# Optimization experiments

Measured on AMD Instinct MI355X. Metric: run time of the kernel, lower is better.

Reference implementation:

```python
import jax, jax.numpy as jnp
import numpy as np

DIM = 256
HEADS = 8


def _ln(x, g, b, eps=1e-5):
    mu = jnp.mean(x, axis=-1, keepdims=True)
    var = jnp.var(x, axis=-1, keepdims=True)
    return (x - mu) * jax.lax.rsqrt(var + eps) * g + b


def setup_inputs() -> dict:
    key = jax.random.key(0)
    ks = jax.random.split(key, 12)
    d = DIM
    s = lambda fan: 1.0 / np.sqrt(fan)
    return {
        "x": jax.random.normal(ks[0], (1, d, 64, 64), dtype=jnp.float32),
        "ln1_g": jnp.ones((d,), jnp.float32),
        "ln1_b": jnp.zeros((d,), jnp.float32),
        "w_qkv": jax.random.normal(ks[1], (3 * d, d), jnp.float32) * s(d),
        "b_qkv": jnp.zeros((3 * d,), jnp.float32),
        "w_proj": jax.random.normal(ks[2], (d, d), jnp.float32) * s(d),
        "b_proj": jnp.zeros((d,), jnp.float32),
        "ln2_g": jnp.ones((d,), jnp.float32),
        "ln2_b": jnp.zeros((d,), jnp.float32),
        "w_mlp1": jax.random.normal(ks[3], (4 * d, d), jnp.float32) * s(d),
        "b_mlp1": jnp.zeros((4 * d,), jnp.float32),
        "w_mlp2": jax.random.normal(ks[4], (d, 4 * d), jnp.float32) * s(4 * d),
        "b_mlp2": jnp.zeros((d,), jnp.float32),
    }


def reference(x, ln1_g, ln1_b, w_qkv, b_qkv, w_proj, b_proj,
              ln2_g, ln2_b, w_mlp1, b_mlp1, w_mlp2, b_mlp2):
    B, C, H, W = x.shape
    hd = HEADS
    d = C // hd
    scale = d ** (-0.5)
    # work channels-last: [B, H, W, C] -> [B, HW, C]
    xl = jnp.transpose(x, (0, 2, 3, 1)).reshape(B, H * W, C)

    # --- attention branch ---
    xn = _ln(xl, ln1_g, ln1_b)
    qkv = jnp.einsum('bnc,oc->bno', xn, w_qkv) + b_qkv  # [B, N, 3C]
    q, k, v = jnp.split(qkv, 3, axis=-1)
    def heads(t):  # [B,N,C] -> [B,h,N,d]
        return jnp.transpose(t.reshape(B, H * W, hd, d), (0, 2, 1, 3))
    q, k, v = heads(q), heads(k), heads(v)
    attn = jax.nn.softmax(jnp.einsum('bhnd,bhmd->bhnm', q, k) * scale, axis=-1)
    out = jnp.einsum('bhnm,bhmd->bhnd', attn, v)  # [B,h,N,d]
    out = jnp.transpose(out, (0, 2, 1, 3)).reshape(B, H * W, C)
    xl = xl + jnp.einsum('bnc,oc->bno', out, w_proj) + b_proj

    # --- MLP branch ---
    xn = _ln(xl, ln2_g, ln2_b)
    h1 = jax.nn.gelu(jnp.einsum('bnc,oc->bno', xn, w_mlp1) + b_mlp1,
                     approximate=False)
    xl = xl + jnp.einsum('bnf,of->bno', h1, w_mlp2) + b_mlp2

    return jnp.transpose(xl.reshape(B, H, W, C), (0, 3, 1, 2))
```

## Files before the change

### kernel.cpp

```cpp
#include <hip/hip_runtime.h>
#include <hip/hip_bf16.h>

typedef __bf16 bf16_t;
typedef __bf16 bf16x8 __attribute__((ext_vector_type(8)));
typedef __bf16 bf16x4 __attribute__((ext_vector_type(4)));
typedef float  f32x4  __attribute__((ext_vector_type(4)));

#define MFMA(a,b,c) __builtin_amdgcn_mfma_f32_16x16x32_bf16((a),(b),(c),0,0,0)

__device__ __forceinline__ size_t pidx(int n, int k, int K) {
  return (size_t)(n >> 4) * (K << 4) + ((k >> 3) << 7) + ((n & 15) << 3) + (k & 7);
}

__global__ __launch_bounds__(256) void cvt_pack_all(const float* __restrict__ w_qkv,
                                                    const float* __restrict__ w_proj,
                                                    const float* __restrict__ w_mlp1,
                                                    const float* __restrict__ w_mlp2,
                                                    bf16_t* __restrict__ wq, bf16_t* __restrict__ wp,
                                                    bf16_t* __restrict__ w1, bf16_t* __restrict__ w2) {
  int b = blockIdx.x;
  const float* src; bf16_t* dst; int t0, ksh;
  if (b < 96)       { src = w_qkv;  dst = wq; ksh = 5; t0 = b * 256; }
  else if (b < 128) { src = w_proj; dst = wp; ksh = 5; t0 = (b - 96) * 256; }
  else if (b < 256) { src = w_mlp1; dst = w1; ksh = 5; t0 = (b - 128) * 256; }
  else              { src = w_mlp2; dst = w2; ksh = 7; t0 = (b - 256) * 256; }
  int t = t0 + threadIdx.x;
  int n = t >> ksh, kb = t & ((1 << ksh) - 1);
  int K = 8 << ksh;
  const float* p = src + (size_t)n * K + kb * 8;
  float4 a = *(const float4*)p;
  float4 c = *(const float4*)(p + 4);
  bf16x8 o = {(bf16_t)a.x, (bf16_t)a.y, (bf16_t)a.z, (bf16_t)a.w,
              (bf16_t)c.x, (bf16_t)c.y, (bf16_t)c.z, (bf16_t)c.w};
  *(bf16x8*)(dst + (size_t)(n >> 4) * (K << 4) + kb * 128 + ((n & 15) << 3)) = o;
}

__global__ __launch_bounds__(256) void fused_in(const float* __restrict__ x,
                                                const float* __restrict__ g,
                                                const float* __restrict__ bta,
                                                float* __restrict__ xl,
                                                bf16_t* __restrict__ xn) {
  __shared__ float tile[256][33];
  __shared__ float psum[8][32], psq[8][32], mu_s[32], rs_s[32];
  int t = threadIdx.x, n0 = blockIdx.x * 32;
  int lane32 = t & 31, grp = t >> 5;
#pragma unroll
  for (int it = 0; it < 32; ++it) {
    int c = grp + it * 8;
    tile[c][lane32] = x[(size_t)c * 4096 + n0 + lane32];
  }
  __syncthreads();
  float s = 0.f, sq = 0.f;
#pragma unroll
  for (int ci = 0; ci < 32; ++ci) {
    float v = tile[grp * 32 + ci][lane32];
    s += v; sq += v * v;
  }
  psum[grp][lane32] = s; psq[grp][lane32] = sq;
  __syncthreads();
  if (t < 32) {
    float S = 0.f, Q = 0.f;
#pragma unroll
    for (int p = 0; p < 8; ++p) { S += psum[p][t]; Q += psq[p][t]; }
    float mu = S * (1.0f / 256.0f);
    float var = Q * (1.0f / 256.0f) - mu * mu;
    mu_s[t] = mu; rs_s[t] = rsqrtf(var + 1e-5f);
  }
  __syncthreads();
  {
    float mu = mu_s[lane32], rs = rs_s[lane32];
    int row = n0 + lane32;
    bf16_t* op = xn + (size_t)(row >> 4) * 4096 + ((row & 15) << 3);
#pragma unroll
    for (int cc8 = 0; cc8 < 4; ++cc8) {
      int c0 = grp * 32 + cc8 * 8;
      bf16x8 o;
#pragma unroll
      for (int j = 0; j < 8; ++j) {
        int c = c0 + j;
        o[j] = (bf16_t)((tile[c][lane32] - mu) * rs * g[c] + bta[c]);
      }
      *(bf16x8*)(op + ((c0 >> 3) << 7)) = o;
    }
  }
#pragma unroll
  for (int it = 0; it < 4; ++it) {
    int j = grp + it * 8;
#pragma unroll
    for (int c0 = 0; c0 < 256; c0 += 32)
      xl[(size_t)(n0 + j) * 256 + c0 + lane32] = tile[c0 + lane32][j];
  }
}

template <int K, int EPI, int RPW, int KS = 1>
__global__ __launch_bounds__(256) void gemm_bt(const bf16_t* __restrict__ A,
                                               const bf16_t* __restrict__ W,
                                               const float* __restrict__ bias,
                                               void* __restrict__ outp, int ldn) {
  constexpr int RB = RPW / 16;
  constexpr int KLEN = K / KS;
  int w = threadIdx.x >> 6, lane = threadIdx.x & 63;
  int quad = lane >> 4, idx = lane & 15;
  int row0 = blockIdx.x * (4 * RPW) + w * RPW;
  int col0 = blockIdx.y * 64;
  int kb0 = (KS > 1) ? blockIdx.z * KLEN : 0;
  f32x4 acc[RB][4];
#pragma unroll
  for (int rb = 0; rb < RB; ++rb)
#pragma unroll
    for (int nb = 0; nb < 4; ++nb) acc[rb][nb] = (f32x4){0.f, 0.f, 0.f, 0.f};
  const bf16_t* abase = A + (size_t)(row0 >> 4) * (K << 4) + quad * 128 + idx * 8;
  const bf16_t* wbase = W + (size_t)(col0 >> 4) * (K << 4) + quad * 128 + idx * 8;
#pragma unroll 4
  for (int k0 = kb0; k0 < kb0 + KLEN; k0 += 32) {
    bf16x8 a[RB];
#pragma unroll
    for (int rb = 0; rb < RB; ++rb)
      a[rb] = *(const bf16x8*)(abase + (size_t)rb * (K << 4) + k0 * 16);
#pragma unroll
    for (int nb = 0; nb < 4; ++nb) {
      bf16x8 b = *(const bf16x8*)(wbase + (size_t)nb * (K << 4) + k0 * 16);
#pragma unroll
      for (int rb = 0; rb < RB; ++rb) acc[rb][nb] = MFMA(a[rb], b, acc[rb][nb]);
    }
  }
#pragma unroll
  for (int nb = 0; nb < 4; ++nb) {
    int c = col0 + nb * 16 + idx;
    float bv = (EPI == 4) ? 0.f : bias[c];
#pragma unroll
    for (int rb = 0; rb < RB; ++rb)
#pragma unroll
      for (int r = 0; r < 4; ++r) {
        int rr = row0 + rb * 16 + quad * 4 + r;
        float v = acc[rb][nb][r] + bv;
        if constexpr (EPI == 1) {
          v = 0.5f * v * (1.0f + erff(v * 0.70710678118654752f));
          ((bf16_t*)outp)[pidx(rr, c, ldn)] = (bf16_t)v;
        } else if constexpr (EPI == 4) {
          ((float*)outp)[((size_t)blockIdx.z * 4096 + rr) * ldn + c] = v;
        } else {
          bf16_t* qh = (bf16_t*)outp;
          bf16_t* kh = qh + 1048576;
          bf16_t* vp = kh + 1048576;
          if (c < 256) {
            qh[(size_t)(c >> 5) * 131072 + rr * 32 + (c & 31)] = (bf16_t)v;
          } else if (c < 512) {
            kh[(size_t)((c - 256) >> 5) * 131072 + rr * 32 + (c & 31)] = (bf16_t)v;
          } else {
            vp[(size_t)((c - 512) >> 5) * 131072 + (rr >> 5) * 1024 + (c & 31) * 32 + (rr & 31)] = (bf16_t)v;
          }
        }
      }
  }
}

#define SPLIT 4
__global__ __launch_bounds__(256, 4) void attn_split(const bf16_t* __restrict__ qkvh,
                                                     bf16_t* __restrict__ o_part,
                                                     float* __restrict__ l_part) {
  __shared__ bf16_t P[4][32][72];
  int w = threadIdx.x >> 6, lane = threadIdx.x & 63;
  int quad = lane >> 4, idx = lane & 15;
  int qt = blockIdx.x & 31;
  int h  = (blockIdx.x >> 5) & 7;
  int sp = blockIdx.x >> 8;
  int qrow = qt * 128 + w * 32;
  const bf16_t* qh = qkvh + (size_t)h * 131072;
  const bf16_t* kh = qh + 8 * 131072;
  const bf16_t* vp = kh + 8 * 131072;
  const float cs = 0.25503518f;
  bf16x8 qr0 = *(const bf16x8*)(qh + (size_t)(qrow + idx) * 32 + quad * 8);
  bf16x8 qr1 = *(const bf16x8*)(qh + (size_t)(qrow + 16 + idx) * 32 + quad * 8);
  bf16x8 qf0, qf1;
#pragma unroll
  for (int j = 0; j < 8; ++j) {
    qf0[j] = (bf16_t)((float)qr0[j] * cs);
    qf1[j] = (bf16_t)((float)qr1[j] * cs);
  }
  float ls0 = 0.f, ls1 = 0.f;
  f32x4 o00 = {0.f,0.f,0.f,0.f}, o01 = {0.f,0.f,0.f,0.f};
  f32x4 o10 = {0.f,0.f,0.f,0.f}, o11 = {0.f,0.f,0.f,0.f};
  const f32x4 zero = {0.f,0.f,0.f,0.f};
  int kbase = sp * 1024;

  bf16x8 kf[4];
#pragma unroll
  for (int kb = 0; kb < 4; ++kb)
    kf[kb] = *(const bf16x8*)(kh + (size_t)(kbase + kb * 16 + idx) * 32 + quad * 8);

  for (int kt = 0; kt < 16; ++kt) {
    int k0 = kbase + kt * 64;
    int k1 = kbase + ((kt + 1) & 15) * 64;
    const bf16_t* vt = vp + (size_t)(k0 >> 5) * 1024 + quad * 8;
    bf16x8 vv0 = *(const bf16x8*)(vt + idx * 32);
    bf16x8 vv1 = *(const bf16x8*)(vt + (idx + 16) * 32);
    bf16x8 vv2 = *(const bf16x8*)(vt + 1024 + idx * 32);
    bf16x8 vv3 = *(const bf16x8*)(vt + 1024 + (idx + 16) * 32);
    bf16x8 kfn[4];
#pragma unroll
    for (int kb = 0; kb < 4; ++kb)
      kfn[kb] = *(const bf16x8*)(kh + (size_t)(k1 + kb * 16 + idx) * 32 + quad * 8);
#pragma unroll
    for (int kb = 0; kb < 4; ++kb) {
      f32x4 s0 = MFMA(kf[kb], qf0, zero);
      f32x4 s1 = MFMA(kf[kb], qf1, zero);
      float a0 = __builtin_amdgcn_exp2f(s0[0]), a1 = __builtin_amdgcn_exp2f(s0[1]);
      float a2 = __builtin_amdgcn_exp2f(s0[2]), a3 = __builtin_amdgcn_exp2f(s0[3]);
      float b0 = __builtin_amdgcn_exp2f(s1[0]), b1 = __builtin_amdgcn_exp2f(s1[1]);
      float b2 = __builtin_amdgcn_exp2f(s1[2]), b3 = __builtin_amdgcn_exp2f(s1[3]);
      ls0 += (a0 + a1) + (a2 + a3);
      ls1 += (b0 + b1) + (b2 + b3);
      bf16x4 pk0 = {(bf16_t)a0, (bf16_t)a1, (bf16_t)a2, (bf16_t)a3};
      bf16x4 pk1 = {(bf16_t)b0, (bf16_t)b1, (bf16_t)b2, (bf16_t)b3};
      *(bf16x4*)&P[w][idx][kb * 16 + quad * 4] = pk0;
      *(bf16x4*)&P[w][16 + idx][kb * 16 + quad * 4] = pk1;
    }
#pragma unroll
    for (int kc = 0; kc < 2; ++kc) {
      bf16x8 pa0 = *(const bf16x8*)&P[w][idx][kc * 32 + quad * 8];
      bf16x8 pa1 = *(const bf16x8*)&P[w][16 + idx][kc * 32 + quad * 8];
      bf16x8 va = kc ? vv2 : vv0;
      bf16x8 vb = kc ? vv3 : vv1;
      o00 = MFMA(pa0, va, o00);
      o01 = MFMA(pa0, vb, o01);
      o10 = MFMA(pa1, va, o10);
      o11 = MFMA(pa1, vb, o11);
    }
#pragma unroll
    for (int kb = 0; kb < 4; ++kb) kf[kb] = kfn[kb];
  }
  ls0 += __shfl_xor(ls0, 16); ls0 += __shfl_xor(ls0, 32);
  ls1 += __shfl_xor(ls1, 16); ls1 += __shfl_xor(ls1, 32);
  if (quad == 0) {
    l_part[((size_t)sp * 8 + h) * 4096 + qrow + idx]      = ls0;
    l_part[((size_t)sp * 8 + h) * 4096 + qrow + 16 + idx] = ls1;
  }
#pragma unroll
  for (int r = 0; r < 4; ++r) {
    int n0 = qrow + quad * 4 + r;
    size_t b0a = ((size_t)sp * 4096 + n0) * 256 + h * 32;
    o_part[b0a + idx]      = (bf16_t)o00[r];
    o_part[b0a + 16 + idx] = (bf16_t)o01[r];
    size_t b1a = b0a + 16 * 256;
    o_part[b1a + idx]      = (bf16_t)o10[r];
    o_part[b1a + 16 + idx] = (bf16_t)o11[r];
  }
}

__global__ __launch_bounds__(256) void attn_norm(const bf16_t* __restrict__ o_part,
                                                 const float* __restrict__ l_part,
                                                 bf16_t* __restrict__ attn) {
  int i = (blockIdx.x * 256 + threadIdx.x) * 4;
  int n = i >> 8, cc = i & 255, h = cc >> 5;
  float l = 0.f;
#pragma unroll
  for (int s = 0; s < SPLIT; ++s) l += l_part[((size_t)s * 8 + h) * 4096 + n];
  float inv = 1.0f / l;
  float acc[4] = {0.f, 0.f, 0.f, 0.f};
#pragma unroll
  for (int s = 0; s < SPLIT; ++s) {
    bf16x4 v = *(const bf16x4*)(o_part + ((size_t)s * 4096 + n) * 256 + cc);
#pragma unroll
    for (int j = 0; j < 4; ++j) acc[j] += (float)v[j];
  }
  bf16x4 o = {(bf16_t)(acc[0] * inv), (bf16_t)(acc[1] * inv),
              (bf16_t)(acc[2] * inv), (bf16_t)(acc[3] * inv)};
  *(bf16x4*)(attn + (size_t)(n >> 4) * 4096 + ((cc >> 3) << 7) + ((n & 15) << 3) + (cc & 7)) = o;
}

__global__ __launch_bounds__(256) void combine_ln(const float* __restrict__ pp,
                                                  const float* __restrict__ xl,
                                                  const float* __restrict__ bias,
                                                  const float* __restrict__ g,
                                                  const float* __restrict__ bta,
                                                  float* __restrict__ xl2,
                                                  bf16_t* __restrict__ xn2) {
  int row  = blockIdx.x * 4 + (threadIdx.x >> 6);
  int lane = threadIdx.x & 63;
  size_t ri = (size_t)row * 64 + lane;
  float4 p0 = ((const float4*)pp)[ri];
  float4 p1 = ((const float4*)pp)[ri + 4096 * 64];
  float4 rr = ((const float4*)xl)[ri];
  float4 bb = ((const float4*)bias)[lane];
  float4 v = {p0.x + p1.x + rr.x + bb.x, p0.y + p1.y + rr.y + bb.y,
              p0.z + p1.z + rr.z + bb.z, p0.w + p1.w + rr.w + bb.w};
  ((float4*)xl2)[ri] = v;
  float s  = v.x + v.y + v.z + v.w;
  float sq = v.x * v.x + v.y * v.y + v.z * v.z + v.w * v.w;
#pragma unroll
  for (int off = 32; off; off >>= 1) {
    s  += __shfl_xor(s, off);
    sq += __shfl_xor(sq, off);
  }
  float mu  = s * (1.0f / 256.0f);
  float var = sq * (1.0f / 256.0f) - mu * mu;
  float rs  = rsqrtf(var + 1e-5f);
  float4 gg = ((const float4*)g)[lane];
  float4 b2 = ((const float4*)bta)[lane];
  bf16x4 o = {(bf16_t)((v.x - mu) * rs * gg.x + b2.x),
              (bf16_t)((v.y - mu) * rs * gg.y + b2.y),
              (bf16_t)((v.z - mu) * rs * gg.z + b2.z),
              (bf16_t)((v.w - mu) * rs * gg.w + b2.w)};
  int k = lane * 4;
  *(bf16x4*)(xn2 + (size_t)(row >> 4) * 4096 + ((k >> 3) << 7) + ((row & 15) << 3) + (k & 7)) = o;
}

__global__ __launch_bounds__(256) void combine_transpose(const float* __restrict__ mp,
                                                         const float* __restrict__ xl2,
                                                         const float* __restrict__ bias,
                                                         float* __restrict__ dst) {
  __shared__ float tile[32][33];
  int n0 = blockIdx.x * 32, c0 = blockIdx.y * 32;
  int a = threadIdx.x & 31, b = threadIdx.x >> 5;
  float bv = bias[c0 + a];
#pragma unroll
  for (int i = 0; i < 4; ++i) {
    int n = b + i * 8;
    size_t base = (size_t)(n0 + n) * 256 + c0 + a;
    float v = xl2[base] + bv;
#pragma unroll
    for (int s = 0; s < 4; ++s) v += mp[(size_t)s * 1048576 + base];
    tile[a][n] = v;
  }
  __syncthreads();
#pragma unroll
  for (int i = 0; i < 4; ++i) {
    int c = b + i * 8;
    dst[(size_t)(c0 + c) * 4096 + n0 + a] = tile[c][a];
  }
}

extern "C" void kernel_launch(void* const* d_in, const int* in_sizes, int n_in,
                              void* d_out, int out_size, void* d_ws, size_t ws_size,
                              hipStream_t stream) {
  const float* x      = (const float*)d_in[0];
  const float* ln1_g  = (const float*)d_in[1];
  const float* ln1_b  = (const float*)d_in[2];
  const float* w_qkv  = (const float*)d_in[3];
  const float* b_qkv  = (const float*)d_in[4];
  const float* w_proj = (const float*)d_in[5];
  const float* b_proj = (const float*)d_in[6];
  const float* ln2_g  = (const float*)d_in[7];
  const float* ln2_b  = (const float*)d_in[8];
  const float* w_mlp1 = (const float*)d_in[9];
  const float* b_mlp1 = (const float*)d_in[10];
  const float* w_mlp2 = (const float*)d_in[11];
  const float* b_mlp2 = (const float*)d_in[12];

  char* ws = (char*)d_ws;
  bf16_t* qkvh   = (bf16_t*)(ws + 0);
  float*  xl     = (float*)(ws + (6u << 20));
  bf16_t* xn     = (bf16_t*)(ws + (10u << 20));
  bf16_t* o_part = (bf16_t*)(ws + (12u << 20));
  bf16_t* attn   = (bf16_t*)(ws + (20u << 20));
  bf16_t* wq     = (bf16_t*)(ws + (22u << 20));
  bf16_t* wp     = wq + 196608;
  bf16_t* w1     = wp + 65536;
  bf16_t* w2     = w1 + 262144;
  float*  l_part = (float*)(ws + (24064u << 10));
  float*  pp     = (float*)(ws + (24u << 20));
  float*  xl2    = (float*)(ws + (10u << 20));
  bf16_t* xn2    = (bf16_t*)(ws + (14u << 20));
  bf16_t* h1     = (bf16_t*)(ws + 0);
  float*  mp     = (float*)(ws + (24u << 20));

  cvt_pack_all<<<384, 256, 0, stream>>>(w_qkv, w_proj, w_mlp1, w_mlp2, wq, wp, w1, w2);
  fused_in<<<128, 256, 0, stream>>>(x, ln1_g, ln1_b, xl, xn);

  gemm_bt<256, 3, 16><<<dim3(64, 12), 256, 0, stream>>>(xn, wq, b_qkv, qkvh, 768);
  attn_split<<<256 * SPLIT, 256, 0, stream>>>(qkvh, o_part, l_part);
  attn_norm<<<1024, 256, 0, stream>>>(o_part, l_part, attn);

  gemm_bt<256, 4, 16, 2><<<dim3(64, 4, 2), 256, 0, stream>>>(attn, wp, nullptr, pp, 256);
  combine_ln<<<1024, 256, 0, stream>>>(pp, xl, b_proj, ln2_g, ln2_b, xl2, xn2);

  gemm_bt<256, 1, 16><<<dim3(64, 16), 256, 0, stream>>>(xn2, w1, b_mlp1, h1, 1024);
  gemm_bt<1024, 4, 16, 4><<<dim3(64, 4, 4), 256, 0, stream>>>(h1, w2, nullptr, mp, 256);
  combine_transpose<<<dim3(128, 8), 256, 0, stream>>>(mp, xl2, b_mlp2, (float*)d_out);
}
```

Before: 169.5 us.

## Software-pipeline attention P tiles, pack o_part stores, tanh-approx GELU, relocate buffers

Attention now double-buffers the P tile in shared memory and computes the next tile's QK^T and exp before the current PV MFMAs, so softmax math overlaps the PV matmuls. Partial outputs are stored as packed bf16 pairs in 32-bit words, and attn_norm reads them with 128-bit loads using half the threads. The erf GELU is replaced with a tanh approximation built from exp2 and rcp, and workspace buffers are moved around. The tanh GELU differs numerically from the exact erf form, and the double buffer doubles shared memory per block.

Measured after the change: 176.8 us. +4.3%, slower.

```diff
diff --git a/kernel.cpp b/kernel.cpp
--- a/kernel.cpp
+++ b/kernel.cpp
@@ -5,11 +5,18 @@
 typedef __bf16 bf16x8 __attribute__((ext_vector_type(8)));
 typedef __bf16 bf16x4 __attribute__((ext_vector_type(4)));
 typedef float  f32x4  __attribute__((ext_vector_type(4)));
+typedef unsigned int uint;
 
 #define MFMA(a,b,c) __builtin_amdgcn_mfma_f32_16x16x32_bf16((a),(b),(c),0,0,0)
 
 __device__ __forceinline__ size_t pidx(int n, int k, int K) {
   return (size_t)(n >> 4) * (K << 4) + ((k >> 3) << 7) + ((n & 15) << 3) + (k & 7);
+}
+
+__device__ __forceinline__ uint packbf2(float lo, float hi) {
+  unsigned short a = __builtin_bit_cast(unsigned short, (bf16_t)lo);
+  unsigned short b = __builtin_bit_cast(unsigned short, (bf16_t)hi);
+  return (uint)a | ((uint)b << 16);
 }
 
 __global__ __launch_bounds__(256) void cvt_pack_all(const float* __restrict__ w_qkv,
@@ -135,7 +142,10 @@
         int rr = row0 + rb * 16 + quad * 4 + r;
         float v = acc[rb][nb][r] + bv;
         if constexpr (EPI == 1) {
-          v = 0.5f * v * (1.0f + erff(v * 0.70710678118654752f));
+          float z = v * (0.7978845608f + 0.0356774081f * v * v);
+          float t = __builtin_amdgcn_exp2f(z * 2.885390082f);
+          float th = 1.f - 2.f * __builtin_amdgcn_rcpf(t + 1.f);
+          v = 0.5f * v * (1.f + th);
           ((bf16_t*)outp)[pidx(rr, c, ldn)] = (bf16_t)v;
         } else if constexpr (EPI == 4) {
           ((float*)outp)[((size_t)blockIdx.z * 4096 + rr) * ldn + c] = v;
@@ -157,9 +167,9 @@
 
 #define SPLIT 4
 __global__ __launch_bounds__(256, 4) void attn_split(const bf16_t* __restrict__ qkvh,
-                                                     bf16_t* __restrict__ o_part,
+                                                     uint* __restrict__ o_part,
                                                      float* __restrict__ l_part) {
-  __shared__ bf16_t P[4][32][72];
+  __shared__ bf16_t P[2][4][32][72];
   int w = threadIdx.x >> 6, lane = threadIdx.x & 63;
   int quad = lane >> 4, idx = lane & 15;
   int qt = blockIdx.x & 31;
@@ -189,44 +199,68 @@
   for (int kb = 0; kb < 4; ++kb)
     kf[kb] = *(const bf16x8*)(kh + (size_t)(kbase + kb * 16 + idx) * 32 + quad * 8);
 
-  for (int kt = 0; kt < 16; ++kt) {
-    int k0 = kbase + kt * 64;
-    int k1 = kbase + ((kt + 1) & 15) * 64;
+#pragma unroll
+  for (int kb = 0; kb < 4; ++kb) {
+    f32x4 s0 = MFMA(kf[kb], qf0, zero);
+    f32x4 s1 = MFMA(kf[kb], qf1, zero);
+    float a0 = __builtin_amdgcn_exp2f(s0[0]), a1 = __builtin_amdgcn_exp2f(s0[1]);
+    float a2 = __builtin_amdgcn_exp2f(s0[2]), a3 = __builtin_amdgcn_exp2f(s0[3]);
+    float b0 = __builtin_amdgcn_exp2f(s1[0]), b1 = __builtin_amdgcn_exp2f(s1[1]);
+    float b2 = __builtin_amdgcn_exp2f(s1[2]), b3 = __builtin_amdgcn_exp2f(s1[3]);
+    ls0 += (a0 + a1) + (a2 + a3);
+    ls1 += (b0 + b1) + (b2 + b3);
+    bf16x4 pk0 = {(bf16_t)a0, (bf16_t)a1, (bf16_t)a2, (bf16_t)a3};
+    bf16x4 pk1 = {(bf16_t)b0, (bf16_t)b1, (bf16_t)b2, (bf16_t)b3};
+    *(bf16x4*)&P[0][w][idx][kb * 16 + quad * 4] = pk0;
+    *(bf16x4*)&P[0][w][16 + idx][kb * 16 + quad * 4] = pk1;
+  }
+#pragma unroll
+  for (int kb = 0; kb < 4; ++kb)
+    kf[kb] = *(const bf16x8*)(kh + (size_t)(kbase + 64 + kb * 16 + idx) * 32 + quad * 8);
+
+#pragma unroll 2
+  for (int t = 0; t < 16; ++t) {
+    int par = t & 1;
+    int k0 = kbase + t * 64;
+    bf16x8 pa00 = *(const bf16x8*)&P[par][w][idx][quad * 8];
+    bf16x8 pa01 = *(const bf16x8*)&P[par][w][idx][32 + quad * 8];
+    bf16x8 pa10 = *(const bf16x8*)&P[par][w][16 + idx][quad * 8];
+    bf16x8 pa11 = *(const bf16x8*)&P[par][w][16 + idx][32 + quad * 8];
     const bf16_t* vt = vp + (size_t)(k0 >> 5) * 1024 + quad * 8;
     bf16x8 vv0 = *(const bf16x8*)(vt + idx * 32);
     bf16x8 vv1 = *(const bf16x8*)(vt + (idx + 16) * 32);
     bf16x8 vv2 = *(const bf16x8*)(vt + 1024 + idx * 32);
     bf16x8 vv3 = *(const bf16x8*)(vt + 1024 + (idx + 16) * 32);
+    int kn = kbase + ((t + 2) & 15) * 64;
     bf16x8 kfn[4];
 #pragma unroll
     for (int kb = 0; kb < 4; ++kb)
-      kfn[kb] = *(const bf16x8*)(kh + (size_t)(k1 + kb * 16 + idx) * 32 + quad * 8);
-#pragma unroll
-    for (int kb = 0; kb < 4; ++kb) {
-      f32x4 s0 = MFMA(kf[kb], qf0, zero);
-      f32x4 s1 = MFMA(kf[kb], qf1, zero);
-      float a0 = __builtin_amdgcn_exp2f(s0[0]), a1 = __builtin_amdgcn_exp2f(s0[1]);
-      float a2 = __builtin_amdgcn_exp2f(s0[2]), a3 = __builtin_amdgcn_exp2f(s0[3]);
-      float b0 = __builtin_amdgcn_exp2f(s1[0]), b1 = __builtin_amdgcn_exp2f(s1[1]);
-      float b2 = __builtin_amdgcn_exp2f(s1[2]), b3 = __builtin_amdgcn_exp2f(s1[3]);
-      ls0 += (a0 + a1) + (a2 + a3);
-      ls1 += (b0 + b1) + (b2 + b3);
-      bf16x4 pk0 = {(bf16_t)a0, (bf16_t)a1, (bf16_t)a2, (bf16_t)a3};
-      bf16x4 pk1 = {(bf16_t)b0, (bf16_t)b1, (bf16_t)b2, (bf16_t)b3};
-      *(bf16x4*)&P[w][idx][kb * 16 + quad * 4] = pk0;
-      *(bf16x4*)&P[w][16 + idx][kb * 16 + quad * 4] = pk1;
+      kfn[kb] = *(const bf16x8*)(kh + (size_t)(kn + kb * 16 + idx) * 32 + quad * 8);
+    if (t < 15) {
+#pragma unroll
+      for (int kb = 0; kb < 4; ++kb) {
+        f32x4 s0 = MFMA(kf[kb], qf0, zero);
+        f32x4 s1 = MFMA(kf[kb], qf1, zero);
+        float a0 = __builtin_amdgcn_exp2f(s0[0]), a1 = __builtin_amdgcn_exp2f(s0[1]);
+        float a2 = __builtin_amdgcn_exp2f(s0[2]), a3 = __builtin_amdgcn_exp2f(s0[3]);
+        float b0 = __builtin_amdgcn_exp2f(s1[0]), b1 = __builtin_amdgcn_exp2f(s1[1]);
+        float b2 = __builtin_amdgcn_exp2f(s1[2]), b3 = __builtin_amdgcn_exp2f(s1[3]);
+        ls0 += (a0 + a1) + (a2 + a3);
+        ls1 += (b0 + b1) + (b2 + b3);
+        bf16x4 pk0 = {(bf16_t)a0, (bf16_t)a1, (bf16_t)a2, (bf16_t)a3};
+        bf16x4 pk1 = {(bf16_t)b0, (bf16_t)b1, (bf16_t)b2, (bf16_t)b3};
+        *(bf16x4*)&P[1 - par][w][idx][kb * 16 + quad * 4] = pk0;
+        *(bf16x4*)&P[1 - par][w][16 + idx][kb * 16 + quad * 4] = pk1;
+      }
     }
-#pragma unroll
-    for (int kc = 0; kc < 2; ++kc) {
-      bf16x8 pa0 = *(const bf16x8*)&P[w][idx][kc * 32 + quad * 8];
-      bf16x8 pa1 = *(const bf16x8*)&P[w][16 + idx][kc * 32 + quad * 8];
-      bf16x8 va = kc ? vv2 : vv0;
-      bf16x8 vb = kc ? vv3 : vv1;
-      o00 = MFMA(pa0, va, o00);
-      o01 = MFMA(pa0, vb, o01);
-      o10 = MFMA(pa1, va, o10);
-      o11 = MFMA(pa1, vb, o11);
-    }
+    o00 = MFMA(pa00, vv0, o00);
+    o01 = MFMA(pa00, vv1, o01);
+    o10 = MFMA(pa10, vv0, o10);
+    o11 = MFMA(pa10, vv1, o11);
+    o00 = MFMA(pa01, vv2, o00);
+    o01 = MFMA(pa01, vv3, o01);
+    o10 = MFMA(pa11, vv2, o10);
+    o11 = MFMA(pa11, vv3, o11);
 #pragma unroll
     for (int kb = 0; kb < 4; ++kb) kf[kb] = kfn[kb];
   }
@@ -239,34 +273,43 @@
 #pragma unroll
   for (int r = 0; r < 4; ++r) {
     int n0 = qrow + quad * 4 + r;
-    size_t b0a = ((size_t)sp * 4096 + n0) * 256 + h * 32;
-    o_part[b0a + idx]      = (bf16_t)o00[r];
-    o_part[b0a + 16 + idx] = (bf16_t)o01[r];
-    size_t b1a = b0a + 16 * 256;
-    o_part[b1a + idx]      = (bf16_t)o10[r];
-    o_part[b1a + 16 + idx] = (bf16_t)o11[r];
-  }
-}
-
-__global__ __launch_bounds__(256) void attn_norm(const bf16_t* __restrict__ o_part,
+    o_part[(((size_t)sp * 4096 + n0) * 8 + h) * 16 + idx] = packbf2(o00[r], o01[r]);
+    int n1 = n0 + 16;
+    o_part[(((size_t)sp * 4096 + n1) * 8 + h) * 16 + idx] = packbf2(o10[r], o11[r]);
+  }
+}
+
+__global__ __launch_bounds__(256) void attn_norm(const uint* __restrict__ o_part,
                                                  const float* __restrict__ l_part,
                                                  bf16_t* __restrict__ attn) {
-  int i = (blockIdx.x * 256 + threadIdx.x) * 4;
-  int n = i >> 8, cc = i & 255, h = cc >> 5;
+  int t = blockIdx.x * 256 + threadIdx.x;
+  int j0 = (t & 3) * 4;
+  int h  = (t >> 2) & 7;
+  int n  = t >> 5;
   float l = 0.f;
 #pragma unroll
   for (int s = 0; s < SPLIT; ++s) l += l_part[((size_t)s * 8 + h) * 4096 + n];
   float inv = 1.0f / l;
-  float acc[4] = {0.f, 0.f, 0.f, 0.f};
+  float alo[4] = {0.f,0.f,0.f,0.f}, ahi[4] = {0.f,0.f,0.f,0.f};
 #pragma unroll
   for (int s = 0; s < SPLIT; ++s) {
-    bf16x4 v = *(const bf16x4*)(o_part + ((size_t)s * 4096 + n) * 256 + cc);
-#pragma unroll
-    for (int j = 0; j < 4; ++j) acc[j] += (float)v[j];
-  }
-  bf16x4 o = {(bf16_t)(acc[0] * inv), (bf16_t)(acc[1] * inv),
-              (bf16_t)(acc[2] * inv), (bf16_t)(acc[3] * inv)};
-  *(bf16x4*)(attn + (size_t)(n >> 4) * 4096 + ((cc >> 3) << 7) + ((n & 15) << 3) + (cc & 7)) = o;
+    const uint* p = o_part + (((size_t)s * 4096 + n) * 8 + h) * 16 + j0;
+    uint4 v = *(const uint4*)p;
+    uint vv[4] = {v.x, v.y, v.z, v.w};
+#pragma unroll
+    for (int jj = 0; jj < 4; ++jj) {
+      alo[jj] += __builtin_bit_cast(float, vv[jj] << 16);
+      ahi[jj] += __builtin_bit_cast(float, vv[jj] & 0xffff0000u);
+    }
+  }
+  bf16x4 lo = {(bf16_t)(alo[0] * inv), (bf16_t)(alo[1] * inv),
+               (bf16_t)(alo[2] * inv), (bf16_t)(alo[3] * inv)};
+  bf16x4 hi = {(bf16_t)(ahi[0] * inv), (bf16_t)(ahi[1] * inv),
+               (bf16_t)(ahi[2] * inv), (bf16_t)(ahi[3] * inv)};
+  int k1 = h * 32 + j0;
+  int k2 = k1 + 16;
+  *(bf16x4*)(attn + (size_t)(n >> 4) * 4096 + ((k1 >> 3) << 7) + ((n & 15) << 3) + (k1 & 7)) = lo;
+  *(bf16x4*)(attn + (size_t)(n >> 4) * 4096 + ((k2 >> 3) << 7) + ((n & 15) << 3) + (k2 & 7)) = hi;
 }
 
 __global__ __launch_bounds__(256) void combine_ln(const float* __restrict__ pp,
@@ -279,12 +322,14 @@
   int row  = blockIdx.x * 4 + (threadIdx.x >> 6);
   int lane = threadIdx.x & 63;
   size_t ri = (size_t)row * 64 + lane;
-  float4 p0 = ((const float4*)pp)[ri];
-  float4 p1 = ((const float4*)pp)[ri + 4096 * 64];
   float4 rr = ((const float4*)xl)[ri];
   float4 bb = ((const float4*)bias)[lane];
-  float4 v = {p0.x + p1.x + rr.x + bb.x, p0.y + p1.y + rr.y + bb.y,
-              p0.z + p1.z + rr.z + bb.z, p0.w + p1.w + rr.w + bb.w};
+  float4 v = {rr.x + bb.x, rr.y + bb.y, rr.z + bb.z, rr.w + bb.w};
+#pragma unroll
+  for (int s = 0; s < 2; ++s) {
+    float4 p = ((const float4*)pp)[ri + (size_t)s * 4096 * 64];
+    v.x += p.x; v.y += p.y; v.z += p.z; v.w += p.w;
+  }
   ((float4*)xl2)[ri] = v;
   float s  = v.x + v.y + v.z + v.w;
   float sq = v.x * v.x + v.y * v.y + v.z * v.z + v.w * v.w;
@@ -352,25 +397,25 @@
   bf16_t* qkvh   = (bf16_t*)(ws + 0);
   float*  xl     = (float*)(ws + (6u << 20));
   bf16_t* xn     = (bf16_t*)(ws + (10u << 20));
-  bf16_t* o_part = (bf16_t*)(ws + (12u << 20));
+  uint*   o_part = (uint*)(ws + (12u << 20));
   bf16_t* attn   = (bf16_t*)(ws + (20u << 20));
-  bf16_t* wq     = (bf16_t*)(ws + (22u << 20));
-  bf16_t* wp     = wq + 196608;
-  bf16_t* w1     = wp + 65536;
-  bf16_t* w2     = w1 + 262144;
-  float*  l_part = (float*)(ws + (24064u << 10));
   float*  pp     = (float*)(ws + (24u << 20));
   float*  xl2    = (float*)(ws + (10u << 20));
   bf16_t* xn2    = (bf16_t*)(ws + (14u << 20));
   bf16_t* h1     = (bf16_t*)(ws + 0);
-  float*  mp     = (float*)(ws + (24u << 20));
+  float*  mp     = (float*)(ws + (16u << 20));
+  bf16_t* wq     = (bf16_t*)(ws + (32u << 20));
+  bf16_t* wp     = wq + 196608;
+  bf16_t* w1     = wp + 65536;
+  bf16_t* w2     = w1 + 262144;
+  float*  l_part = (float*)(ws + (34304u << 10));
 
   cvt_pack_all<<<384, 256, 0, stream>>>(w_qkv, w_proj, w_mlp1, w_mlp2, wq, wp, w1, w2);
   fused_in<<<128, 256, 0, stream>>>(x, ln1_g, ln1_b, xl, xn);
 
   gemm_bt<256, 3, 16><<<dim3(64, 12), 256, 0, stream>>>(xn, wq, b_qkv, qkvh, 768);
   attn_split<<<256 * SPLIT, 256, 0, stream>>>(qkvh, o_part, l_part);
-  attn_norm<<<1024, 256, 0, stream>>>(o_part, l_part, attn);
+  attn_norm<<<512, 256, 0, stream>>>(o_part, l_part, attn);
 
   gemm_bt<256, 4, 16, 2><<<dim3(64, 4, 2), 256, 0, stream>>>(attn, wp, nullptr, pp, 256);
   combine_ln<<<1024, 256, 0, stream>>>(pp, xl, b_proj, ln2_g, ln2_b, xl2, xn2);
```
